# Kernel optimization log

Measured on AMD Instinct MI355X. Metric: run time of the kernel, lower is better.

## Reference

```python
import jax, jax.numpy as jnp
import numpy as np

TEMP = 0.07
EPS = 1e-6
NORM_EPS = 1e-12  # F.normalize default eps
LN_EPS = 1e-5

B, D, H, W = 32, 256, 64, 64
K = 256
DFF = 2048


def _l2norm(v, axis):
    n = jnp.sqrt(jnp.sum(v * v, axis=axis, keepdims=True))
    return v / jnp.maximum(n, NORM_EPS)


def _layernorm(v, g, b):
    mu = jnp.mean(v, axis=-1, keepdims=True)
    var = jnp.mean((v - mu) ** 2, axis=-1, keepdims=True)
    return (v - mu) * jax.lax.rsqrt(var + LN_EPS) * g + b


def setup_inputs() -> dict:
    key = jax.random.key(0)
    ks = jax.random.split(key, 8)
    s1 = 1.0 / np.sqrt(D)
    s2 = 1.0 / np.sqrt(DFF)
    return {
        "x": jax.random.normal(ks[0], (B, D, H, W), jnp.float32),
        "tgt": jax.random.normal(ks[1], (B, K, D), jnp.float32),
        "w1": jax.random.uniform(ks[2], (DFF, D), jnp.float32, -s1, s1),
        "b1": jax.random.uniform(ks[3], (DFF,), jnp.float32, -s1, s1),
        "w2": jax.random.uniform(ks[4], (D, DFF), jnp.float32, -s2, s2),
        "b2": jax.random.uniform(ks[5], (D,), jnp.float32, -s2, s2),
        "g2": jnp.ones((D,), jnp.float32),
        "be2": jnp.zeros((D,), jnp.float32),
        "g3": jnp.ones((D,), jnp.float32),
        "be3": jnp.zeros((D,), jnp.float32),
    }


def reference(x, tgt, w1, b1, w2, b2, g2, be2, g3, be3):
    # slot cross-attention with L2-normalized q/k
    tn = _l2norm(tgt, axis=2)           # (b,k,d)
    xn = _l2norm(x, axis=1)             # (b,d,h,w)
    dots = jnp.einsum('bkd,bdhw->bkhw', tn, xn)
    attn = jax.nn.softmax(dots / TEMP, axis=1) + EPS          # softmax over slots
    attn = attn / jnp.sum(attn, axis=(2, 3), keepdims=True)   # spatial normalization
    tgt2 = jnp.einsum('bdhw,bkhw->bkd', x, attn)
    t = _layernorm(tgt + tgt2, g2, be2)
    # FFN (dropout = identity in eval)
    ff = jnp.maximum(t @ w1.T + b1, 0.0) @ w2.T + b2
    return _layernorm(t + ff, g3, be3)
```

## Files before the change

kernel.cpp:

```cpp
#include <hip/hip_runtime.h>
#include <hip/hip_bf16.h>

using bf16 = __hip_bfloat16;

typedef __attribute__((ext_vector_type(8))) short short8;
typedef __attribute__((ext_vector_type(4))) float f32x4;

constexpr int Bb = 32, Dd = 256, HWw = 4096, Kk = 256, Ff = 2048;
constexpr float TEMP_INV = 1.0f / 0.07f;
constexpr float EPSf = 1e-6f;
constexpr float NORM_EPSf = 1e-12f;
constexpr float LN_EPSf = 1e-5f;

static __device__ __forceinline__ float b2f(bf16 v) { return __bfloat162float(v); }
static __device__ __forceinline__ bf16 f2b(float v) { return __float2bfloat16(v); }


__global__ __launch_bounds__(64) void k_tn(const float* __restrict__ tgt,
                                           bf16* __restrict__ tnbf) {
  int row = blockIdx.x;
  int b = row >> 8, slot = row & 255;
  int lane = threadIdx.x;
  const float* src = tgt + (size_t)row * Dd + lane * 4;
  float v[4];
#pragma unroll
  for (int u = 0; u < 4; u++) v[u] = src[u];
  float ss = v[0] * v[0] + v[1] * v[1] + v[2] * v[2] + v[3] * v[3];
#pragma unroll
  for (int m = 32; m >= 1; m >>= 1) ss += __shfl_xor(ss, m, 64);
  float inv = 1.0f / fmaxf(sqrtf(ss), NORM_EPSf);
  bf16 o[4] __attribute__((aligned(8)));
#pragma unroll
  for (int u = 0; u < 4; u++) o[u] = f2b(v[u] * inv);
  int s = lane >> 3;
  int q2 = (lane >> 1) & 3;
  int jh = (lane & 1) * 4;
  size_t fi = (size_t)((slot >> 4) * 64 + q2 * 16 + (slot & 15));
  *(float2*)(tnbf + ((size_t)(b * 8 + s) * 1024 + fi) * 8 + jh) = *(float2*)o;
}

__global__ __launch_bounds__(64) void k_prew1(const float* __restrict__ w1,
                                              bf16* __restrict__ w1bf) {
  int f = blockIdx.x;
  int lane = threadIdx.x;
  const float* src = w1 + (size_t)f * Dd + lane * 4;
  bf16 o[4] __attribute__((aligned(8)));
#pragma unroll
  for (int u = 0; u < 4; u++) o[u] = f2b(src[u]);
  int s = lane >> 3;
  int q2 = (lane >> 1) & 3;
  int jh = (lane & 1) * 4;
  size_t fi = (size_t)(((f & 63) >> 4) * 64 + q2 * 16 + (f & 15));
  *(float2*)(w1bf + ((size_t)((f >> 6) * 8 + s) * 256 + fi) * 8 + jh) = *(float2*)o;
}

__global__ __launch_bounds__(64) void k_prew2(const float* __restrict__ w2,
                                              bf16* __restrict__ w2bf) {
  int d = blockIdx.x;
  int lane = threadIdx.x;
  const float* src = w2 + (size_t)d * Ff + lane * 32;
  size_t gbase = (size_t)((d >> 6) * 64 + lane) * 256;
  int fbase = ((d & 63) >> 4) * 64 + (d & 15);
#pragma unroll
  for (int q2 = 0; q2 < 4; q2++) {
    float4 v0 = *(const float4*)(src + q2 * 8);
    float4 v1 = *(const float4*)(src + q2 * 8 + 4);
    bf16 o[8] __attribute__((aligned(16)));
    o[0] = f2b(v0.x); o[1] = f2b(v0.y); o[2] = f2b(v0.z); o[3] = f2b(v0.w);
    o[4] = f2b(v1.x); o[5] = f2b(v1.y); o[6] = f2b(v1.z); o[7] = f2b(v1.w);
    *(float4*)(w2bf + (gbase + fbase + q2 * 16) * 8) = *(float4*)o;
  }
}

#define MFMA16(a, b, c) __builtin_amdgcn_mfma_f32_16x16x32_bf16(a, b, c, 0, 0, 0)

__global__ __launch_bounds__(256) void k_dots(const bf16* __restrict__ tnbf,
                                              const float* __restrict__ x,
                                              bf16* __restrict__ xb,
                                              bf16* __restrict__ attn_t,
                                              float* __restrict__ S) {
  __shared__ __align__(16) bf16 Bs[2][4 * 520];
  __shared__ float ssred[64 * 17];
  __shared__ float nxl[64];
  __shared__ float red[512];
  int b = blockIdx.x >> 6;
  int hw0 = (blockIdx.x & 63) * 64;
  int tid = threadIdx.x;
  int wave = tid >> 6, lane = tid & 63;
  int quad = lane >> 4, nl = lane & 15;

  int dp = tid >> 4;
  int ch = tid & 15;
  int qb = dp >> 2;
  int jb = (dp & 3) * 2;

  f32x4 acc[4][4];
#pragma unroll
  for (int i = 0; i < 4; i++)
#pragma unroll
    for (int j = 0; j < 4; j++) acc[i][j] = (f32x4){0.f, 0.f, 0.f, 0.f};
  float ssp[4] = {0.f, 0.f, 0.f, 0.f};

  for (int s = 0; s < 8; s++) {
    bf16* bsb = &Bs[s & 1][0];
    {
      const float* xr = x + (size_t)((b << 8) + s * 32 + 2 * dp) * HWw + hw0 + ch * 4;
      float4 va = *(const float4*)xr;
      float4 vb = *(const float4*)(xr + HWw);
      float vva[4] = {va.x, va.y, va.z, va.w};
      float vvb[4] = {vb.x, vb.y, vb.z, vb.w};
      bf16 pa[4] __attribute__((aligned(8)));
      bf16 pb[4] __attribute__((aligned(8)));
#pragma unroll
      for (int jj = 0; jj < 4; jj++) {
        ssp[jj] += vva[jj] * vva[jj] + vvb[jj] * vvb[jj];
        pa[jj] = f2b(vva[jj]);
        pb[jj] = f2b(vvb[jj]);
      }
      bf16* xw = xb + (size_t)((b << 8) + s * 32 + 2 * dp) * HWw + hw0 + ch * 4;
      *(float2*)xw = *(float2*)pa;
      *(float2*)(xw + HWw) = *(float2*)pb;
#pragma unroll
      for (int jj = 0; jj < 4; jj++) {
        int hwl = ch * 4 + jj;
        int nt = hwl >> 4;
        int li = (qb << 4) | (hwl & 15);
        union { bf16 h[2]; unsigned int u; } pk;
        pk.h[0] = pa[jj];
        pk.h[1] = pb[jj];
        *(unsigned int*)&bsb[nt * 520 + li * 8 + jb] = pk.u;
      }
    }
    __syncthreads();
    const bf16* tsrc = tnbf + (size_t)(b * 8 + s) * 1024 * 8;
    short8 af[4], bfv[4];
#pragma unroll
    for (int mt = 0; mt < 4; mt++)
      af[mt] = *(const short8*)(tsrc + (size_t)(((wave << 2) + mt) * 64 + lane) * 8);
#pragma unroll
    for (int nt = 0; nt < 4; nt++)
      bfv[nt] = *(const short8*)(bsb + nt * 520 + lane * 8);
#pragma unroll
    for (int mt = 0; mt < 4; mt++)
#pragma unroll
      for (int nt = 0; nt < 4; nt++) acc[mt][nt] = MFMA16(af[mt], bfv[nt], acc[mt][nt]);
  }

#pragma unroll
  for (int jj = 0; jj < 4; jj++) ssred[(ch * 4 + jj) * 17 + dp] = ssp[jj];
  __syncthreads();
  if (tid < 64) {
    float sum = 0.f;
#pragma unroll
    for (int i = 0; i < 16; i++) sum += ssred[tid * 17 + i];
    nxl[tid] = TEMP_INV / fmaxf(sqrtf(sum), NORM_EPSf);
  }
  __syncthreads();

  float sc[4];
#pragma unroll
  for (int nt = 0; nt < 4; nt++) sc[nt] = nxl[nt * 16 + nl];
#pragma unroll
  for (int mt = 0; mt < 4; mt++)
#pragma unroll
    for (int nt = 0; nt < 4; nt++)
#pragma unroll
      for (int r = 0; r < 4; r++) acc[mt][nt][r] *= sc[nt];

  float* red2 = red + 256;

  float pmax[4];
#pragma unroll
  for (int nt = 0; nt < 4; nt++) {
    float m = acc[0][nt][0];
#pragma unroll
    for (int mt = 0; mt < 4; mt++)
#pragma unroll
      for (int r = 0; r < 4; r++) m = fmaxf(m, acc[mt][nt][r]);
    m = fmaxf(m, __shfl_xor(m, 16, 64));
    m = fmaxf(m, __shfl_xor(m, 32, 64));
    pmax[nt] = m;
  }
  if (lane < 16) {
#pragma unroll
    for (int nt = 0; nt < 4; nt++) red[((wave << 2) + nt) * 16 + nl] = pmax[nt];
  }
  __syncthreads();
  float cmax[4];
#pragma unroll
  for (int nt = 0; nt < 4; nt++) {
    float m = red[nt * 16 + nl];
#pragma unroll
    for (int w2 = 1; w2 < 4; w2++) m = fmaxf(m, red[((w2 << 2) + nt) * 16 + nl]);
    cmax[nt] = m;
  }

  float psum[4];
#pragma unroll
  for (int nt = 0; nt < 4; nt++) {
    float s = 0.f;
#pragma unroll
    for (int mt = 0; mt < 4; mt++)
#pragma unroll
      for (int r = 0; r < 4; r++) {
        float e = __expf(acc[mt][nt][r] - cmax[nt]);
        acc[mt][nt][r] = e;
        s += e;
      }
    s += __shfl_xor(s, 16, 64);
    s += __shfl_xor(s, 32, 64);
    psum[nt] = s;
  }
  if (lane < 16) {
#pragma unroll
    for (int nt = 0; nt < 4; nt++) red2[((wave << 2) + nt) * 16 + nl] = psum[nt];
  }
  __syncthreads();
  float ci[4];
#pragma unroll
  for (int nt = 0; nt < 4; nt++) {
    float s = 0.f;
#pragma unroll
    for (int w2 = 0; w2 < 4; w2++) s += red2[((w2 << 2) + nt) * 16 + nl];
    ci[nt] = 1.0f / s;
  }

#pragma unroll
  for (int mt = 0; mt < 4; mt++) {
    int slotg = (b << 8) + (wave << 6) + (mt << 4) + (quad << 2);
#pragma unroll
    for (int r = 0; r < 4; r++) {
      size_t base = (size_t)(slotg + r) * HWw + hw0;
      float rs = 0.f;
#pragma unroll
      for (int nt = 0; nt < 4; nt++) {
        float a = acc[mt][nt][r] * ci[nt] + EPSf;
        bf16 hb = f2b(a);
        attn_t[base + nt * 16 + nl] = hb;
        rs += b2f(hb);
      }
      rs += __shfl_xor(rs, 1, 64);
      rs += __shfl_xor(rs, 2, 64);
      rs += __shfl_xor(rs, 4, 64);
      rs += __shfl_xor(rs, 8, 64);
      if (nl == 0) atomicAdd(&S[slotg + r], rs);
    }
  }
}

static __device__ __forceinline__ void stage_bf16_tile(const bf16* __restrict__ src, int ld,
                                                       bf16* __restrict__ dst, int tid) {
  int r = (tid & 15) | ((tid >> 6) << 4);
  int q = (tid >> 4) & 3;
  float4 v = *(const float4*)(src + (size_t)r * ld + q * 8);
  *(float4*)(dst + (size_t)(((r >> 4) << 6) | (q << 4) | (r & 15)) * 8) = v;
}

__global__ __launch_bounds__(256) void k_gemm2(const bf16* __restrict__ attn_t,
                                               const bf16* __restrict__ xb,
                                               float* __restrict__ t2) {
  __shared__ __align__(16) bf16 As[64 * 32];
  __shared__ __align__(16) bf16 Bsf[64 * 32];
  int n = blockIdx.x;
  int b = n & 31;
  int tile = n >> 5;
  int d0 = (tile & 3) * 64;
  int k0 = ((tile >> 2) & 3) * 64;
  int h0b = (tile >> 4) * 1024;
  int tid = threadIdx.x;
  int wave = tid >> 6, lane = tid & 63;
  int am = (wave >> 1) * 2, bn = (wave & 1) * 2;

  f32x4 acc[2][2];
#pragma unroll
  for (int i = 0; i < 2; i++)
#pragma unroll
    for (int j = 0; j < 2; j++) acc[i][j] = (f32x4){0.f, 0.f, 0.f, 0.f};

  const bf16* Ap = attn_t + (size_t)((b << 8) + k0) * HWw + h0b;
  const bf16* Bp = xb + (size_t)((b << 8) + d0) * HWw + h0b;
  for (int h0 = 0; h0 < 1024; h0 += 32) {
    stage_bf16_tile(Ap + h0, HWw, As, tid);
    stage_bf16_tile(Bp + h0, HWw, Bsf, tid);
    __syncthreads();
    short8 af[2], bfr[2];
#pragma unroll
    for (int i = 0; i < 2; i++) af[i] = *(const short8*)(As + (size_t)((am + i) * 64 + lane) * 8);
#pragma unroll
    for (int j = 0; j < 2; j++) bfr[j] = *(const short8*)(Bsf + (size_t)((bn + j) * 64 + lane) * 8);
#pragma unroll
    for (int i = 0; i < 2; i++)
#pragma unroll
      for (int j = 0; j < 2; j++) acc[i][j] = MFMA16(af[i], bfr[j], acc[i][j]);
    __syncthreads();
  }
  int quad = lane >> 4, nl = lane & 15;
#pragma unroll
  for (int i = 0; i < 2; i++)
#pragma unroll
    for (int r = 0; r < 4; r++) {
      int row = (b << 8) + k0 + (am + i) * 16 + quad * 4 + r;
#pragma unroll
      for (int j = 0; j < 2; j++) {
        int col = d0 + (bn + j) * 16 + nl;
        atomicAdd(&t2[(size_t)row * Dd + col], acc[i][j][r]);
      }
    }
}

__global__ __launch_bounds__(64) void k_ln_pre(const float* __restrict__ t2,
                                               const float* __restrict__ S,
                                               const float* __restrict__ tgt,
                                               const float* __restrict__ g,
                                               const float* __restrict__ be,
                                               float* __restrict__ t,
                                               bf16* __restrict__ tbf) {
  int row = blockIdx.x;
  int lane = threadIdx.x;
  float sInv = 1.0f / S[row];
  const float* p2 = t2 + (size_t)row * Dd + lane * 4;
  const float* pt = tgt + (size_t)row * Dd + lane * 4;
  float v[4];
#pragma unroll
  for (int u = 0; u < 4; u++) v[u] = p2[u] * sInv + pt[u];
  float s1 = v[0] + v[1] + v[2] + v[3];
  float s2 = v[0] * v[0] + v[1] * v[1] + v[2] * v[2] + v[3] * v[3];
#pragma unroll
  for (int m = 32; m >= 1; m >>= 1) {
    s1 += __shfl_xor(s1, m, 64);
    s2 += __shfl_xor(s2, m, 64);
  }
  float mu = s1 * (1.0f / 256.0f);
  float var = s2 * (1.0f / 256.0f) - mu * mu;
  float rs = rsqrtf(fmaxf(var, 0.f) + LN_EPSf);
  float* po = t + (size_t)row * Dd + lane * 4;
  bf16 o[4] __attribute__((aligned(8)));
#pragma unroll
  for (int u = 0; u < 4; u++) {
    float val = (v[u] - mu) * rs * g[lane * 4 + u] + be[lane * 4 + u];
    po[u] = val;
    o[u] = f2b(val);
  }
  int s = lane >> 3;
  int q2 = (lane >> 1) & 3;
  int jh = (lane & 1) * 4;
  size_t fi = (size_t)(((row & 63) >> 4) * 64 + q2 * 16 + (row & 15));
  *(float2*)(tbf + ((size_t)((row >> 6) * 8 + s) * 256 + fi) * 8 + jh) = *(float2*)o;
}

__global__ __launch_bounds__(256) void k_ffn1(const bf16* __restrict__ tbf,
                                              const bf16* __restrict__ w1bf,
                                              const float* __restrict__ b1,
                                              bf16* __restrict__ h1) {
  int rowgrp = blockIdx.x >> 5;
  int fgrp = blockIdx.x & 31;
  int tid = threadIdx.x;
  int wave = tid >> 6, lane = tid & 63;
  int am = (wave >> 1) * 2, bn = (wave & 1) * 2;

  f32x4 acc[2][2];
#pragma unroll
  for (int i = 0; i < 2; i++)
#pragma unroll
    for (int j = 0; j < 2; j++) acc[i][j] = (f32x4){0.f, 0.f, 0.f, 0.f};

  const bf16* Abase = tbf + (size_t)rowgrp * 8 * 256 * 8;
  const bf16* Bbase = w1bf + (size_t)fgrp * 8 * 256 * 8;
#pragma unroll
  for (int s = 0; s < 8; s++) {
    short8 af[2], bfr[2];
#pragma unroll
    for (int i = 0; i < 2; i++)
      af[i] = *(const short8*)(Abase + ((size_t)s * 256 + ((am + i) * 64 + lane)) * 8);
#pragma unroll
    for (int j = 0; j < 2; j++)
      bfr[j] = *(const short8*)(Bbase + ((size_t)s * 256 + ((bn + j) * 64 + lane)) * 8);
#pragma unroll
    for (int i = 0; i < 2; i++)
#pragma unroll
      for (int j = 0; j < 2; j++) acc[i][j] = MFMA16(af[i], bfr[j], acc[i][j]);
  }
  int quad = lane >> 4, nl = lane & 15;
  int row0 = rowgrp * 64, f0 = fgrp * 64;
#pragma unroll
  for (int j = 0; j < 2; j++) {
    int f = f0 + (bn + j) * 16 + nl;
    float bias = b1[f];
#pragma unroll
    for (int i = 0; i < 2; i++)
#pragma unroll
      for (int r = 0; r < 4; r++) {
        int row = row0 + (am + i) * 16 + quad * 4 + r;
        h1[(size_t)row * Ff + f] = f2b(fmaxf(acc[i][j][r] + bias, 0.f));
      }
  }
}

__global__ __launch_bounds__(256) void k_ffn2(const bf16* __restrict__ h1,
                                              const bf16* __restrict__ w2bf,
                                              float* __restrict__ o2) {
  __shared__ __align__(16) bf16 As[64 * 32];
  int n = blockIdx.x;
  int rowgrp = n >> 4;
  int dgrp = (n >> 2) & 3;
  int ksp = n & 3;
  int tid = threadIdx.x;
  int wave = tid >> 6, lane = tid & 63;
  int am = (wave >> 1) * 2, bn = (wave & 1) * 2;

  f32x4 acc[2][2];
#pragma unroll
  for (int i = 0; i < 2; i++)
#pragma unroll
    for (int j = 0; j < 2; j++) acc[i][j] = (f32x4){0.f, 0.f, 0.f, 0.f};

  const bf16* Ap = h1 + (size_t)(rowgrp * 64) * Ff + ksp * 512;
  const bf16* Bbase = w2bf + (size_t)dgrp * 64 * 256 * 8;
  for (int st = 0; st < 16; st++) {
    int sg = ksp * 16 + st;
    stage_bf16_tile(Ap + st * 32, Ff, As, tid);
    __syncthreads();
    short8 af[2], bfr[2];
#pragma unroll
    for (int i = 0; i < 2; i++) af[i] = *(const short8*)(As + (size_t)((am + i) * 64 + lane) * 8);
#pragma unroll
    for (int j = 0; j < 2; j++)
      bfr[j] = *(const short8*)(Bbase + ((size_t)sg * 256 + ((bn + j) * 64 + lane)) * 8);
#pragma unroll
    for (int i = 0; i < 2; i++)
#pragma unroll
      for (int j = 0; j < 2; j++) acc[i][j] = MFMA16(af[i], bfr[j], acc[i][j]);
    __syncthreads();
  }
  int quad = lane >> 4, nl = lane & 15;
#pragma unroll
  for (int i = 0; i < 2; i++)
#pragma unroll
    for (int r = 0; r < 4; r++) {
      int row = rowgrp * 64 + (am + i) * 16 + quad * 4 + r;
#pragma unroll
      for (int j = 0; j < 2; j++) {
        int col = dgrp * 64 + (bn + j) * 16 + nl;
        atomicAdd(&o2[(size_t)row * Dd + col], acc[i][j][r]);
      }
    }
}

__global__ __launch_bounds__(64) void k_ln_out(const float* __restrict__ o2,
                                               const float* __restrict__ b2v,
                                               const float* __restrict__ t,
                                               const float* __restrict__ g,
                                               const float* __restrict__ be,
                                               float* __restrict__ out) {
  int row = blockIdx.x;
  int lane = threadIdx.x;
  const float* po = o2 + (size_t)row * Dd + lane * 4;
  const float* pt = t + (size_t)row * Dd + lane * 4;
  float v[4];
#pragma unroll
  for (int u = 0; u < 4; u++) v[u] = po[u] + b2v[lane * 4 + u] + pt[u];
  float s1 = v[0] + v[1] + v[2] + v[3];
  float s2 = v[0] * v[0] + v[1] * v[1] + v[2] * v[2] + v[3] * v[3];
#pragma unroll
  for (int m = 32; m >= 1; m >>= 1) {
    s1 += __shfl_xor(s1, m, 64);
    s2 += __shfl_xor(s2, m, 64);
  }
  float mu = s1 * (1.0f / 256.0f);
  float var = s2 * (1.0f / 256.0f) - mu * mu;
  float rs = rsqrtf(fmaxf(var, 0.f) + LN_EPSf);
  float* pw = out + (size_t)row * Dd + lane * 4;
#pragma unroll
  for (int u = 0; u < 4; u++)
    pw[u] = (v[u] - mu) * rs * g[lane * 4 + u] + be[lane * 4 + u];
}

extern "C" void kernel_launch(void* const* d_in, const int* in_sizes, int n_in,
                              void* d_out, int out_size, void* d_ws, size_t ws_size,
                              hipStream_t stream) {
  const float* x = (const float*)d_in[0];
  const float* tgt = (const float*)d_in[1];
  const float* w1 = (const float*)d_in[2];
  const float* b1 = (const float*)d_in[3];
  const float* w2 = (const float*)d_in[4];
  const float* b2v = (const float*)d_in[5];
  const float* g2 = (const float*)d_in[6];
  const float* be2 = (const float*)d_in[7];
  const float* g3 = (const float*)d_in[8];
  const float* be3 = (const float*)d_in[9];
  float* out = (float*)d_out;

  char* w = (char*)d_ws;
  bf16* tnbf = (bf16*)w;     w += (size_t)Bb * Kk * Dd * 2;
  float* S = (float*)w;      w += (size_t)Bb * Kk * 4;
  float* t = (float*)w;      w += (size_t)Bb * Kk * Dd * 4;
  float* t2 = (float*)w;     w += (size_t)Bb * Kk * Dd * 4;
  bf16* attn_t = (bf16*)w;   w += (size_t)Bb * HWw * Kk * 2;
  bf16* h1 = (bf16*)w;       w += (size_t)Bb * Kk * Ff * 2;
  bf16* xb = (bf16*)w;       w += (size_t)Bb * Dd * HWw * 2;

  bf16* tbf = tnbf;
  float* o2 = t2;
  bf16* w1bf = attn_t;
  bf16* w2bf = attn_t + (size_t)Ff * Dd;

  hipMemsetAsync(S, 0, (size_t)Bb * Kk * 4, stream);
  hipMemsetAsync(t2, 0, (size_t)Bb * Kk * Dd * 4, stream);
  k_tn<<<Bb * Kk, 64, 0, stream>>>(tgt, tnbf);
  k_dots<<<Bb * (HWw / 64), 256, 0, stream>>>(tnbf, x, xb, attn_t, S);
  k_gemm2<<<Bb * 64, 256, 0, stream>>>(attn_t, xb, t2);
  k_prew1<<<Ff, 64, 0, stream>>>(w1, w1bf);
  k_prew2<<<Dd, 64, 0, stream>>>(w2, w2bf);
  k_ln_pre<<<Bb * Kk, 64, 0, stream>>>(t2, S, tgt, g2, be2, t, tbf);
  hipMemsetAsync(o2, 0, (size_t)Bb * Kk * Dd * 4, stream);
  k_ffn1<<<(Bb * Kk / 64) * (Ff / 64), 256, 0, stream>>>(tbf, w1bf, b1, h1);
  k_ffn2<<<(Bb * Kk / 64) * 16, 256, 0, stream>>>(h1, w2bf, o2);
  k_ln_out<<<Bb * Kk, 64, 0, stream>>>(o2, b2v, t, g3, be3, out);
}
```

Baseline: 460.4 us.

## Prefetch next-stage loads in k_dots and enlarge per-wave tiles in gemm2 and ffn2

```diff
diff --git a/kernel.cpp b/kernel.cpp
--- a/kernel.cpp
+++ b/kernel.cpp
@@ -101,12 +101,21 @@
     for (int j = 0; j < 4; j++) acc[i][j] = (f32x4){0.f, 0.f, 0.f, 0.f};
   float ssp[4] = {0.f, 0.f, 0.f, 0.f};
 
+  float4 va, vb;
+  short8 afp[4];
+  {
+    const float* xr0 = x + (size_t)((b << 8) + 2 * dp) * HWw + hw0 + ch * 4;
+    va = *(const float4*)xr0;
+    vb = *(const float4*)(xr0 + HWw);
+    const bf16* ts0 = tnbf + (size_t)(b * 8) * 1024 * 8;
+#pragma unroll
+    for (int mt = 0; mt < 4; mt++)
+      afp[mt] = *(const short8*)(ts0 + (size_t)(((wave << 2) + mt) * 64 + lane) * 8);
+  }
+
   for (int s = 0; s < 8; s++) {
     bf16* bsb = &Bs[s & 1][0];
     {
-      const float* xr = x + (size_t)((b << 8) + s * 32 + 2 * dp) * HWw + hw0 + ch * 4;
-      float4 va = *(const float4*)xr;
-      float4 vb = *(const float4*)(xr + HWw);
       float vva[4] = {va.x, va.y, va.z, va.w};
       float vvb[4] = {vb.x, vb.y, vb.z, vb.w};
       bf16 pa[4] __attribute__((aligned(8)));
@@ -132,11 +141,19 @@
       }
     }
     __syncthreads();
-    const bf16* tsrc = tnbf + (size_t)(b * 8 + s) * 1024 * 8;
-    short8 af[4], bfv[4];
-#pragma unroll
-    for (int mt = 0; mt < 4; mt++)
-      af[mt] = *(const short8*)(tsrc + (size_t)(((wave << 2) + mt) * 64 + lane) * 8);
+    short8 af[4];
+#pragma unroll
+    for (int mt = 0; mt < 4; mt++) af[mt] = afp[mt];
+    if (s < 7) {
+      const float* xr = x + (size_t)((b << 8) + (s + 1) * 32 + 2 * dp) * HWw + hw0 + ch * 4;
+      va = *(const float4*)xr;
+      vb = *(const float4*)(xr + HWw);
+      const bf16* tsrc = tnbf + (size_t)(b * 8 + s + 1) * 1024 * 8;
+#pragma unroll
+      for (int mt = 0; mt < 4; mt++)
+        afp[mt] = *(const short8*)(tsrc + (size_t)(((wave << 2) + mt) * 64 + lane) * 8);
+    }
+    short8 bfv[4];
 #pragma unroll
     for (int nt = 0; nt < 4; nt++)
       bfv[nt] = *(const short8*)(bsb + nt * 520 + lane * 8);
@@ -259,51 +276,55 @@
 __global__ __launch_bounds__(256) void k_gemm2(const bf16* __restrict__ attn_t,
                                                const bf16* __restrict__ xb,
                                                float* __restrict__ t2) {
-  __shared__ __align__(16) bf16 As[64 * 32];
-  __shared__ __align__(16) bf16 Bsf[64 * 32];
+  __shared__ __align__(16) bf16 As2[2][64 * 32];
+  __shared__ __align__(16) bf16 Bs2[2][64 * 32];
   int n = blockIdx.x;
   int b = n & 31;
-  int tile = n >> 5;
-  int d0 = (tile & 3) * 64;
-  int k0 = ((tile >> 2) & 3) * 64;
-  int h0b = (tile >> 4) * 1024;
+  int r2 = n >> 5;
+  int k0 = (r2 & 1) * 128;
+  int d0 = ((r2 >> 1) & 1) * 128;
+  int h0b = (r2 >> 2) * 512;
   int tid = threadIdx.x;
   int wave = tid >> 6, lane = tid & 63;
-  int am = (wave >> 1) * 2, bn = (wave & 1) * 2;
-
-  f32x4 acc[2][2];
-#pragma unroll
-  for (int i = 0; i < 2; i++)
-#pragma unroll
-    for (int j = 0; j < 2; j++) acc[i][j] = (f32x4){0.f, 0.f, 0.f, 0.f};
+  int wr = wave >> 1, wc = wave & 1;
+
+  f32x4 acc[4][4];
+#pragma unroll
+  for (int i = 0; i < 4; i++)
+#pragma unroll
+    for (int j = 0; j < 4; j++) acc[i][j] = (f32x4){0.f, 0.f, 0.f, 0.f};
 
   const bf16* Ap = attn_t + (size_t)((b << 8) + k0) * HWw + h0b;
   const bf16* Bp = xb + (size_t)((b << 8) + d0) * HWw + h0b;
-  for (int h0 = 0; h0 < 1024; h0 += 32) {
-    stage_bf16_tile(Ap + h0, HWw, As, tid);
-    stage_bf16_tile(Bp + h0, HWw, Bsf, tid);
+  for (int h0 = 0; h0 < 512; h0 += 32) {
+    stage_bf16_tile(Ap + h0, HWw, As2[0], tid);
+    stage_bf16_tile(Ap + (size_t)64 * HWw + h0, HWw, As2[1], tid);
+    stage_bf16_tile(Bp + h0, HWw, Bs2[0], tid);
+    stage_bf16_tile(Bp + (size_t)64 * HWw + h0, HWw, Bs2[1], tid);
     __syncthreads();
-    short8 af[2], bfr[2];
-#pragma unroll
-    for (int i = 0; i < 2; i++) af[i] = *(const short8*)(As + (size_t)((am + i) * 64 + lane) * 8);
-#pragma unroll
-    for (int j = 0; j < 2; j++) bfr[j] = *(const short8*)(Bsf + (size_t)((bn + j) * 64 + lane) * 8);
-#pragma unroll
-    for (int i = 0; i < 2; i++)
-#pragma unroll
-      for (int j = 0; j < 2; j++) acc[i][j] = MFMA16(af[i], bfr[j], acc[i][j]);
+    short8 af[4], bfr[4];
+#pragma unroll
+    for (int mt = 0; mt < 4; mt++)
+      af[mt] = *(const short8*)(&As2[wr][(size_t)(mt * 64 + lane) * 8]);
+#pragma unroll
+    for (int nt = 0; nt < 4; nt++)
+      bfr[nt] = *(const short8*)(&Bs2[wc][(size_t)(nt * 64 + lane) * 8]);
+#pragma unroll
+    for (int mt = 0; mt < 4; mt++)
+#pragma unroll
+      for (int nt = 0; nt < 4; nt++) acc[mt][nt] = MFMA16(af[mt], bfr[nt], acc[mt][nt]);
     __syncthreads();
   }
   int quad = lane >> 4, nl = lane & 15;
 #pragma unroll
-  for (int i = 0; i < 2; i++)
+  for (int mt = 0; mt < 4; mt++)
 #pragma unroll
     for (int r = 0; r < 4; r++) {
-      int row = (b << 8) + k0 + (am + i) * 16 + quad * 4 + r;
-#pragma unroll
-      for (int j = 0; j < 2; j++) {
-        int col = d0 + (bn + j) * 16 + nl;
-        atomicAdd(&t2[(size_t)row * Dd + col], acc[i][j][r]);
+      int row = (b << 8) + k0 + wr * 64 + mt * 16 + quad * 4 + r;
+#pragma unroll
+      for (int nt = 0; nt < 4; nt++) {
+        int col = d0 + wc * 64 + nt * 16 + nl;
+        atomicAdd(&t2[(size_t)row * Dd + col], acc[mt][nt][r]);
       }
     }
 }
@@ -401,47 +422,46 @@
                                               float* __restrict__ o2) {
   __shared__ __align__(16) bf16 As[64 * 32];
   int n = blockIdx.x;
-  int rowgrp = n >> 4;
-  int dgrp = (n >> 2) & 3;
-  int ksp = n & 3;
+  int rowgrp = n >> 3;
+  int ksp = n & 7;
   int tid = threadIdx.x;
   int wave = tid >> 6, lane = tid & 63;
-  int am = (wave >> 1) * 2, bn = (wave & 1) * 2;
-
-  f32x4 acc[2][2];
-#pragma unroll
-  for (int i = 0; i < 2; i++)
-#pragma unroll
-    for (int j = 0; j < 2; j++) acc[i][j] = (f32x4){0.f, 0.f, 0.f, 0.f};
-
-  const bf16* Ap = h1 + (size_t)(rowgrp * 64) * Ff + ksp * 512;
-  const bf16* Bbase = w2bf + (size_t)dgrp * 64 * 256 * 8;
-  for (int st = 0; st < 16; st++) {
-    int sg = ksp * 16 + st;
+
+  f32x4 acc[4][4];
+#pragma unroll
+  for (int i = 0; i < 4; i++)
+#pragma unroll
+    for (int j = 0; j < 4; j++) acc[i][j] = (f32x4){0.f, 0.f, 0.f, 0.f};
+
+  const bf16* Ap = h1 + (size_t)(rowgrp * 64) * Ff + ksp * 256;
+  const bf16* Bbase = w2bf + (size_t)(wave * 64) * 256 * 8;
+  for (int st = 0; st < 8; st++) {
+    int sg = ksp * 8 + st;
     stage_bf16_tile(Ap + st * 32, Ff, As, tid);
     __syncthreads();
-    short8 af[2], bfr[2];
-#pragma unroll
-    for (int i = 0; i < 2; i++) af[i] = *(const short8*)(As + (size_t)((am + i) * 64 + lane) * 8);
-#pragma unroll
-    for (int j = 0; j < 2; j++)
-      bfr[j] = *(const short8*)(Bbase + ((size_t)sg * 256 + ((bn + j) * 64 + lane)) * 8);
-#pragma unroll
-    for (int i = 0; i < 2; i++)
-#pragma unroll
-      for (int j = 0; j < 2; j++) acc[i][j] = MFMA16(af[i], bfr[j], acc[i][j]);
+    short8 af[4], bfr[4];
+#pragma unroll
+    for (int mt = 0; mt < 4; mt++)
+      af[mt] = *(const short8*)(As + (size_t)(mt * 64 + lane) * 8);
+#pragma unroll
+    for (int nt = 0; nt < 4; nt++)
+      bfr[nt] = *(const short8*)(Bbase + ((size_t)sg * 256 + (nt * 64 + lane)) * 8);
+#pragma unroll
+    for (int mt = 0; mt < 4; mt++)
+#pragma unroll
+      for (int nt = 0; nt < 4; nt++) acc[mt][nt] = MFMA16(af[mt], bfr[nt], acc[mt][nt]);
     __syncthreads();
   }
   int quad = lane >> 4, nl = lane & 15;
 #pragma unroll
-  for (int i = 0; i < 2; i++)
+  for (int mt = 0; mt < 4; mt++)
 #pragma unroll
     for (int r = 0; r < 4; r++) {
-      int row = rowgrp * 64 + (am + i) * 16 + quad * 4 + r;
-#pragma unroll
-      for (int j = 0; j < 2; j++) {
-        int col = dgrp * 64 + (bn + j) * 16 + nl;
-        atomicAdd(&o2[(size_t)row * Dd + col], acc[i][j][r]);
+      int row = rowgrp * 64 + mt * 16 + quad * 4 + r;
+#pragma unroll
+      for (int nt = 0; nt < 4; nt++) {
+        int col = wave * 64 + nt * 16 + nl;
+        atomicAdd(&o2[(size_t)row * Dd + col], acc[mt][nt][r]);
       }
     }
 }
@@ -508,12 +528,12 @@
   hipMemsetAsync(t2, 0, (size_t)Bb * Kk * Dd * 4, stream);
   k_tn<<<Bb * Kk, 64, 0, stream>>>(tgt, tnbf);
   k_dots<<<Bb * (HWw / 64), 256, 0, stream>>>(tnbf, x, xb, attn_t, S);
-  k_gemm2<<<Bb * 64, 256, 0, stream>>>(attn_t, xb, t2);
+  k_gemm2<<<1024, 256, 0, stream>>>(attn_t, xb, t2);
   k_prew1<<<Ff, 64, 0, stream>>>(w1, w1bf);
   k_prew2<<<Dd, 64, 0, stream>>>(w2, w2bf);
   k_ln_pre<<<Bb * Kk, 64, 0, stream>>>(t2, S, tgt, g2, be2, t, tbf);
   hipMemsetAsync(o2, 0, (size_t)Bb * Kk * Dd * 4, stream);
   k_ffn1<<<(Bb * Kk / 64) * (Ff / 64), 256, 0, stream>>>(tbf, w1bf, b1, h1);
-  k_ffn2<<<(Bb * Kk / 64) * 16, 256, 0, stream>>>(h1, w2bf, o2);
+  k_ffn2<<<(Bb * Kk / 64) * 8, 256, 0, stream>>>(h1, w2bf, o2);
   k_ln_out<<<Bb * Kk, 64, 0, stream>>>(o2, b2v, t, g3, be3, out);
 }
```

Measured after the change: 460.1 us. About the same (-0.1%).
